# Optimization experiments

Hardware: AMD Instinct MI355X
Metric: run time of the kernel (lower is better)

The kernel has to match this reference:

```python
import jax, jax.numpy as jnp
import numpy as np

N, D = 8192, 128
NUM_CLASSES = 512
LA, UA, K, S, LAMBDA_G, MARGIN = 10.0, 110.0, 3.0, 30.0, 1.0, 0.0


def setup_inputs() -> dict:
    key = jax.random.key(0)
    k1, k2, k3 = jax.random.split(key, 3)
    feat = jax.random.normal(k1, (N, D), dtype=jnp.float32)
    uc = jax.random.uniform(k2, (N,), dtype=jnp.float32)
    label = jax.random.randint(k3, (N,), 0, NUM_CLASSES, dtype=jnp.int64)
    return {"feat": feat, "uc": uc, "label": label}


def _safe_sqrt(d2):
    # matches torch cdist subgradient: grad 0 at exactly-zero distance
    pos = d2 > 0
    return jnp.where(pos, jnp.sqrt(jnp.where(pos, d2, 1.0)), 0.0)


def reference(feat, uc, label):
    # --- norm regularizer g (reg_type='exp_3') ---
    norms = jnp.linalg.norm(feat, axis=-1)                      # [N]
    nx = (norms - LA) / (UA - LA)
    ug = 2.7183 ** (-K)
    reg = ((jnp.exp(-nx * K) / K + ug * nx) / (1.0 - ug)).mean() * LAMBDA_G

    mask = label[:, None] == label[None, :]                      # [N, N] bool

    # normalize=True branch: unit-normalize then euclidean cdist
    f = feat / jnp.maximum(norms, 1e-12)[:, None]                # F.normalize
    gram = f @ f.T                                               # [N, N]
    d2 = jnp.clip(2.0 - 2.0 * gram, 0.0, None)
    similarity = -_safe_sqrt(d2)                                 # -cdist

    uc_pair = uc[:, None] + uc[None, :]
    correction = jnp.where(mask, -(uc_pair - MARGIN), uc_pair)

    similarity = jnp.arcsin(similarity / 2.0) * 2.0 - correction # convert_dist

    maskf = mask.astype(similarity.dtype)
    nmaskf = 1.0 - maskf
    s_pos = -similarity * maskf - 10.0 * nmaskf
    s_neg = similarity * nmaskf - 10.0 * maskf

    logit_p = jax.nn.logsumexp(s_pos * S, axis=-1)               # [N]
    logit_n = jax.nn.logsumexp(s_neg * S, axis=-1)               # [N]
    loss = jax.nn.softplus(logit_p + logit_n).mean()

    # forward returns loss/s + (reg - reg.detach()) (value == loss/s)
    out = loss / S + (reg - jax.lax.stop_gradient(reg))
    return out
```

## Files before the change

### kernel.cpp

```cpp
#include <hip/hip_runtime.h>
#include <hip/hip_bf16.h>
#include <stdint.h>

#define N_ROWS 8192
#define DIM 128
#define NCLS 512
#define NCHUNK 16
#define CHUNK 512
#define JT 32
#define ROUNDS (CHUNK / JT)

#define S2D 43.2808512266689
#define PI2D 1.5707963267948966
#define CN 56.0f
#define CP 16.0f

typedef __attribute__((ext_vector_type(8))) short bf16x8;
typedef __attribute__((ext_vector_type(4))) float f32x4;


__device__ __forceinline__ unsigned short bf16_rne(float f) {
  uint32_t u = __float_as_uint(f);
  u += 0x7FFFu + ((u >> 16) & 1u);
  return (unsigned short)(u >> 16);
}
__device__ __forceinline__ float bf16_f(unsigned short h) {
  return __uint_as_float(((uint32_t)h) << 16);
}

__device__ __forceinline__ float acos_fast(float x) {
  float ax = fabsf(x);
  float p = fmaf(ax, -0.0012624911f, 0.0066700901f);
  p = fmaf(ax, p, -0.0170881256f);
  p = fmaf(ax, p, 0.0308918810f);
  p = fmaf(ax, p, -0.0501743046f);
  p = fmaf(ax, p, 0.0889789874f);
  p = fmaf(ax, p, -0.2145988016f);
  p = fmaf(ax, p, 1.5707963050f);
  float r = sqrtf(1.0f - ax) * p;
  return x >= 0.0f ? r : 3.14159265358979f - r;
}

__device__ __forceinline__ void gload16(const void* g, void* l) {
  __builtin_amdgcn_global_load_lds(
      (__attribute__((address_space(1))) void*)(void*)g,
      (__attribute__((address_space(3))) void*)l, 16, 0, 0);
}


__global__ __launch_bounds__(256) void prep_kernel(const float* __restrict__ feat,
                                                   const int* __restrict__ label,
                                                   unsigned short* __restrict__ fhi,
                                                   unsigned short* __restrict__ flo,
                                                   int* __restrict__ cls_start,
                                                   int* __restrict__ cls_idx) {
  __shared__ int cnt[NCLS];
  __shared__ int ofs[NCLS];
  const int t = threadIdx.x;
  const int w = t >> 6, l = t & 63;

  int row = blockIdx.x * 4 + w;
  float2 v = *(const float2*)(feat + (size_t)row * DIM + l * 2);
  float ss = v.x * v.x + v.y * v.y;
  #pragma unroll
  for (int m = 32; m; m >>= 1) ss += __shfl_xor(ss, m);
  float scale = 1.0f / fmaxf(sqrtf(ss), 1e-12f);
  float fx = v.x * scale, fy = v.y * scale;
  unsigned short hx = bf16_rne(fx), hy = bf16_rne(fy);
  unsigned short lx = bf16_rne(fx - bf16_f(hx)), ly = bf16_rne(fy - bf16_f(hy));
  *(ushort2*)(fhi + (size_t)row * DIM + l * 2) = make_ushort2(hx, hy);
  *(ushort2*)(flo + (size_t)row * DIM + l * 2) = make_ushort2(lx, ly);

  if (blockIdx.x == 0) {
    for (int i = t; i < NCLS; i += 256) cnt[i] = 0;
    __syncthreads();
    for (int i = t; i < N_ROWS; i += 256) atomicAdd(&cnt[label[i]], 1);
    __syncthreads();
    if (t < 64) {
      int loc[8];
      int base = 0;
      #pragma unroll
      for (int b = 0; b < 8; ++b) { loc[b] = base; base += cnt[l * 8 + b]; }
      int v2 = base;
      #pragma unroll
      for (int off = 1; off < 64; off <<= 1) {
        int n = __shfl_up(v2, off);
        if (l >= off) v2 += n;
      }
      int ex = v2 - base;
      #pragma unroll
      for (int b = 0; b < 8; ++b) {
        int s = ex + loc[b];
        ofs[l * 8 + b] = s;
        cls_start[l * 8 + b] = s;
      }
      if (l == 63) cls_start[NCLS] = ex + base;
    }
    __syncthreads();
    for (int i = t; i < N_ROWS; i += 256) {
      int c = label[i];
      int p = atomicAdd(&ofs[c], 1);
      cls_idx[p] = i;
    }
  }
}


__global__ __launch_bounds__(256, 5) void pair_kernel(const unsigned short* __restrict__ fhi,
                                                      const unsigned short* __restrict__ flo,
                                                      const float* __restrict__ uc,
                                                      const int* __restrict__ label,
                                                      float* __restrict__ partial) {
  __shared__ __attribute__((aligned(16))) char smem[2 * 16384];
  constexpr float S2 = (float)S2D;
  constexpr float S2PI2 = (float)(S2D * PI2D);
  constexpr float A0 = (float)(1.0 * S2D);
  constexpr float A1 = (float)(1.0 / 6.0 * S2D);
  constexpr float A2 = (float)(3.0 / 40.0 * S2D);
  constexpr float A3 = (float)(15.0 / 336.0 * S2D);
  constexpr float A4 = (float)(105.0 / 3456.0 * S2D);

  const int t = threadIdx.x;
  const int w = t >> 6, l = t & 63;
  const int lr = l & 15, lg = l >> 4;

  const int lin = blockIdx.y * 128 + blockIdx.x;
  const int dat = (lin & 7) * 256 + (lin >> 3);
  const int i0 = (dat & 127) * 64;
  const int chunk = dat >> 7;

  const char* fhb = (const char*)fhi;
  const char* flb = (const char*)flo;

  bf16x8 a_hi[4], a_lo[4];
  {
    int arow = i0 + w * 16 + lr;
    #pragma unroll
    for (int kk = 0; kk < 4; ++kk) {
      int off = arow * 256 + kk * 64 + lg * 16;
      a_hi[kk] = *(const bf16x8*)(fhb + off);
      a_lo[kk] = *(const bf16x8*)(flb + off);
    }
  }

  int li[4]; float K0[4];
  #pragma unroll
  for (int q = 0; q < 4; ++q) {
    int r = i0 + w * 16 + lg * 4 + q;
    li[q] = label[r];
    K0[q] = CN - S2PI2 - uc[r] * S2;
  }

  float sn[4] = {0.f, 0.f, 0.f, 0.f};

  const int sw = (lr & 7) << 4;
  const int bb = lr * 256 + ((lg * 16) ^ (sw & 0x30));
  int koff[4];
  #pragma unroll
  for (int kk = 0; kk < 4; ++kk) koff[kk] = (kk * 64) ^ (sw & 0x40);

  int rc[2];
  #pragma unroll
  for (int c = 0; c < 2; ++c) {
    int aoff = c * 4096 + t * 16;
    int row = aoff >> 8;
    int off = aoff & 255;
    rc[c] = row * 256 + (off ^ ((row & 7) << 4));
  }
  const int ldst = w * 1024;

  size_t goff = (size_t)chunk * CHUNK * 256;

  #pragma unroll
  for (int c = 0; c < 2; ++c) {
    gload16(fhb + goff + rc[c], smem + c * 4096 + ldst);
    gload16(flb + goff + rc[c], smem + 8192 + c * 4096 + ldst);
  }
  __syncthreads();

  int cur = 0;
  for (int r = 0; r < ROUNDS; ++r) {
    const int j0 = chunk * CHUNK + r * JT;
    int lj_r[2]; float us_r[2];
    #pragma unroll
    for (int sub = 0; sub < 2; ++sub) {
      int j = j0 + sub * 16 + lr;
      lj_r[sub] = label[j];
      us_r[sub] = uc[j] * S2;
    }
    if (r + 1 < ROUNDS) {
      char* nb = smem + (cur ^ 1) * 16384;
      size_t g2 = goff + JT * 256;
      #pragma unroll
      for (int c = 0; c < 2; ++c) {
        gload16(fhb + g2 + rc[c], nb + c * 4096 + ldst);
        gload16(flb + g2 + rc[c], nb + 8192 + c * 4096 + ldst);
      }
    }

    const char* cb_ = smem + cur * 16384;
    #pragma unroll
    for (int sub = 0; sub < 2; ++sub) {
      f32x4 aA = {0.f,0.f,0.f,0.f}, aB = {0.f,0.f,0.f,0.f}, aC = {0.f,0.f,0.f,0.f};
      #pragma unroll
      for (int kk = 0; kk < 4; ++kk) {
        const char* ba = cb_ + bb + koff[kk] + sub * 4096;
        bf16x8 bh = *(const bf16x8*)(ba);
        bf16x8 bl = *(const bf16x8*)(ba + 8192);
        aA = __builtin_amdgcn_mfma_f32_16x16x32_bf16(a_hi[kk], bh, aA, 0, 0, 0);
        aB = __builtin_amdgcn_mfma_f32_16x16x32_bf16(a_hi[kk], bl, aB, 0, 0, 0);
        aC = __builtin_amdgcn_mfma_f32_16x16x32_bf16(a_lo[kk], bh, aC, 0, 0, 0);
      }
      f32x4 acc = (aA + aB) + aC;

      const int lj = lj_r[sub];
      const float us = us_r[sub];
      #pragma unroll
      for (int q = 0; q < 4; ++q) {
        float g = acc[q];
        float u = g * g;
        float p = fmaf(u, A4, A3);
        p = fmaf(u, p, A2);
        p = fmaf(u, p, A1);
        p = fmaf(u, p, A0);
        float vn = fmaf(g, p, K0[q] - us);
        vn = (li[q] == lj) ? -1e30f : vn;
        sn[q] += __builtin_amdgcn_exp2f(vn);
      }
    }
    __syncthreads();
    goff += JT * 256;
    cur ^= 1;
  }

  #pragma unroll
  for (int q = 0; q < 4; ++q) {
    #pragma unroll
    for (int msk = 1; msk < 16; msk <<= 1) sn[q] += __shfl_xor(sn[q], msk);
  }
  if (lr == 0) {
    #pragma unroll
    for (int q = 0; q < 4; ++q) {
      int r = i0 + w * 16 + lg * 4 + q;
      partial[(size_t)r * NCHUNK + chunk] = sn[q];
    }
  }
}


__global__ __launch_bounds__(256) void finalize_kernel(const unsigned short* __restrict__ fhi,
                                                       const unsigned short* __restrict__ flo,
                                                       const float* __restrict__ uc,
                                                       const int* __restrict__ label,
                                                       const float* __restrict__ partial,
                                                       const int* __restrict__ cls_start,
                                                       const int* __restrict__ cls_idx,
                                                       float* __restrict__ blocksum) {
  constexpr float S2 = (float)S2D;
  __shared__ float wsum[4];
  const int t = threadIdx.x;
  const int w = t >> 6, l = t & 63;
  const int row = blockIdx.x * 4 + w;

  float sn = (l < NCHUNK) ? partial[(size_t)row * NCHUNK + l] : 0.f;
  #pragma unroll
  for (int m = 32; m; m >>= 1) sn += __shfl_xor(sn, m);

  ushort2 hi2 = *(const ushort2*)(fhi + (size_t)row * DIM + l * 2);
  ushort2 lo2 = *(const ushort2*)(flo + (size_t)row * DIM + l * 2);
  float fx = bf16_f(hi2.x) + bf16_f(lo2.x);
  float fy = bf16_f(hi2.y) + bf16_f(lo2.y);

  const int c = label[row];
  const int ks = cls_start[c], ke = cls_start[c + 1];
  const float uci = uc[row];
  float sp = 0.f;
  for (int k = ks; k < ke; ++k) {
    int j = cls_idx[k];
    ushort2 hj = *(const ushort2*)(fhi + (size_t)j * DIM + l * 2);
    ushort2 lj = *(const ushort2*)(flo + (size_t)j * DIM + l * 2);
    float g = fx * (bf16_f(hj.x) + bf16_f(lj.x)) + fy * (bf16_f(hj.y) + bf16_f(lj.y));
    #pragma unroll
    for (int m = 32; m; m >>= 1) g += __shfl_xor(g, m);
    g = fminf(1.0f, fmaxf(-1.0f, g));
    float th = acos_fast(g);
    float vp = fmaf(S2, th, -S2 * (uci + uc[j]) - CP);
    sp += __builtin_amdgcn_exp2f(vp);
  }

  float z2 = log2f(sp) + log2f(sn) + (CP - CN);
  float z = 0.69314718056f * z2;
  float v = (z > 20.f) ? z : log1pf(__expf(z));

  if (l == 0) wsum[w] = v;
  __syncthreads();
  if (t == 0) blocksum[blockIdx.x] = wsum[0] + wsum[1] + wsum[2] + wsum[3];
}


__global__ __launch_bounds__(256) void finalize2_kernel(const float* __restrict__ blocksum,
                                                        float* __restrict__ out) {
  __shared__ float w4[4];
  int t = threadIdx.x;
  float s = 0.f;
  #pragma unroll
  for (int k = 0; k < 8; ++k) s += blocksum[t + k * 256];
  #pragma unroll
  for (int m = 32; m; m >>= 1) s += __shfl_xor(s, m);
  if ((t & 63) == 0) w4[t >> 6] = s;
  __syncthreads();
  if (t == 0) out[0] = (w4[0] + w4[1] + w4[2] + w4[3]) * (1.0f / (8192.0f * 30.0f));
}


extern "C" void kernel_launch(void* const* d_in, const int* in_sizes, int n_in,
                              void* d_out, int out_size, void* d_ws, size_t ws_size,
                              hipStream_t stream) {
  const float* feat = (const float*)d_in[0];
  const float* uc   = (const float*)d_in[1];
  const int*   label = (const int*)d_in[2];
  float* out = (float*)d_out;
  char* ws = (char*)d_ws;

  unsigned short* fhi = (unsigned short*)ws;
  unsigned short* flo = (unsigned short*)(ws + (size_t)N_ROWS * DIM * 2);
  float* partial = (float*)(ws + (size_t)N_ROWS * DIM * 4);
  char* p2 = ws + (size_t)N_ROWS * DIM * 4 + (size_t)N_ROWS * NCHUNK * 4;
  int* cls_start = (int*)p2;
  int* cls_idx = (int*)(p2 + 2048 + 64);
  float* blocksum = (float*)(p2 + 2048 + 64 + 32768);

  prep_kernel<<<N_ROWS / 4, 256, 0, stream>>>(feat, label, fhi, flo, cls_start, cls_idx);
  pair_kernel<<<dim3(128, 16), 256, 0, stream>>>(fhi, flo, uc, label, partial);
  finalize_kernel<<<N_ROWS / 4, 256, 0, stream>>>(fhi, flo, uc, label, partial,
                                                  cls_start, cls_idx, blocksum);
  finalize2_kernel<<<1, 256, 0, stream>>>(blocksum, out);
}
```

Baseline: 167.9 us.

## Exploit pairwise symmetry: compute only lower-triangular tiles with column-sum atomics

The negative-pair term is symmetric in i and j, so the pair kernel now launches only tiles on or below the diagonal (1088 instead of 2048). Strictly off-diagonal tiles also reduce their exponentials across rows and atomically add them into a per-column sum, which finalize adds to each row's partial sums. This roughly halves the MFMA and exp work, but adds per-subtile shuffles, global atomics, a memset, and a load imbalance from the triangular tile mapping.

```diff
diff --git a/kernel.cpp b/kernel.cpp
--- a/kernel.cpp
+++ b/kernel.cpp
@@ -9,6 +9,7 @@
 #define CHUNK 512
 #define JT 32
 #define ROUNDS (CHUNK / JT)
+#define NTILES 1088
 
 #define S2D 43.2808512266689
 #define PI2D 1.5707963267948966
@@ -110,7 +111,8 @@
                                                       const unsigned short* __restrict__ flo,
                                                       const float* __restrict__ uc,
                                                       const int* __restrict__ label,
-                                                      float* __restrict__ partial) {
+                                                      float* __restrict__ partial,
+                                                      float* __restrict__ colsum) {
   __shared__ __attribute__((aligned(16))) char smem[2 * 16384];
   constexpr float S2 = (float)S2D;
   constexpr float S2PI2 = (float)(S2D * PI2D);
@@ -124,10 +126,16 @@
   const int w = t >> 6, l = t & 63;
   const int lr = l & 15, lg = l >> 4;
 
-  const int lin = blockIdx.y * 128 + blockIdx.x;
-  const int dat = (lin & 7) * 256 + (lin >> 3);
-  const int i0 = (dat & 127) * 64;
-  const int chunk = dat >> 7;
+  int c = 0;
+  {
+    int rem = blockIdx.x;
+    while (true) { int cnt = 128 - 8 * c; if (rem < cnt) break; rem -= cnt; ++c; }
+    c = (c << 16) | rem;
+  }
+  const int chunk = c >> 16;
+  const int t_ = 8 * chunk + (c & 0xFFFF);
+  const int i0 = t_ * 64;
+  const bool strict = (t_ >= 8 * chunk + 8);
 
   const char* fhb = (const char*)fhi;
   const char* flb = (const char*)flo;
@@ -161,20 +169,20 @@
 
   int rc[2];
   #pragma unroll
-  for (int c = 0; c < 2; ++c) {
-    int aoff = c * 4096 + t * 16;
+  for (int cc = 0; cc < 2; ++cc) {
+    int aoff = cc * 4096 + t * 16;
     int row = aoff >> 8;
     int off = aoff & 255;
-    rc[c] = row * 256 + (off ^ ((row & 7) << 4));
+    rc[cc] = row * 256 + (off ^ ((row & 7) << 4));
   }
   const int ldst = w * 1024;
 
   size_t goff = (size_t)chunk * CHUNK * 256;
 
   #pragma unroll
-  for (int c = 0; c < 2; ++c) {
-    gload16(fhb + goff + rc[c], smem + c * 4096 + ldst);
-    gload16(flb + goff + rc[c], smem + 8192 + c * 4096 + ldst);
+  for (int cc = 0; cc < 2; ++cc) {
+    gload16(fhb + goff + rc[cc], smem + cc * 4096 + ldst);
+    gload16(flb + goff + rc[cc], smem + 8192 + cc * 4096 + ldst);
   }
   __syncthreads();
 
@@ -192,9 +200,9 @@
       char* nb = smem + (cur ^ 1) * 16384;
       size_t g2 = goff + JT * 256;
       #pragma unroll
-      for (int c = 0; c < 2; ++c) {
-        gload16(fhb + g2 + rc[c], nb + c * 4096 + ldst);
-        gload16(flb + g2 + rc[c], nb + 8192 + c * 4096 + ldst);
+      for (int cc = 0; cc < 2; ++cc) {
+        gload16(fhb + g2 + rc[cc], nb + cc * 4096 + ldst);
+        gload16(flb + g2 + rc[cc], nb + 8192 + cc * 4096 + ldst);
       }
     }
 
@@ -215,6 +223,7 @@
 
       const int lj = lj_r[sub];
       const float us = us_r[sub];
+      float e[4];
       #pragma unroll
       for (int q = 0; q < 4; ++q) {
         float g = acc[q];
@@ -225,7 +234,14 @@
         p = fmaf(u, p, A0);
         float vn = fmaf(g, p, K0[q] - us);
         vn = (li[q] == lj) ? -1e30f : vn;
-        sn[q] += __builtin_amdgcn_exp2f(vn);
+        e[q] = __builtin_amdgcn_exp2f(vn);
+        sn[q] += e[q];
+      }
+      if (strict) {
+        float cs = (e[0] + e[1]) + (e[2] + e[3]);
+        cs += __shfl_xor(cs, 16);
+        cs += __shfl_xor(cs, 32);
+        if (l < 16) atomicAdd(&colsum[j0 + sub * 16 + l], cs);
       }
     }
     __syncthreads();
@@ -253,6 +269,7 @@
                                                        const float* __restrict__ uc,
                                                        const int* __restrict__ label,
                                                        const float* __restrict__ partial,
+                                                       const float* __restrict__ colsum,
                                                        const int* __restrict__ cls_start,
                                                        const int* __restrict__ cls_idx,
                                                        float* __restrict__ blocksum) {
@@ -261,10 +278,12 @@
   const int t = threadIdx.x;
   const int w = t >> 6, l = t & 63;
   const int row = blockIdx.x * 4 + w;
-
-  float sn = (l < NCHUNK) ? partial[(size_t)row * NCHUNK + l] : 0.f;
+  const int c_r = row >> 9;
+
+  float sn = (l <= c_r) ? partial[(size_t)row * NCHUNK + l] : 0.f;
   #pragma unroll
   for (int m = 32; m; m >>= 1) sn += __shfl_xor(sn, m);
+  sn += colsum[row];
 
   ushort2 hi2 = *(const ushort2*)(fhi + (size_t)row * DIM + l * 2);
   ushort2 lo2 = *(const ushort2*)(flo + (size_t)row * DIM + l * 2);
@@ -329,10 +348,12 @@
   int* cls_start = (int*)p2;
   int* cls_idx = (int*)(p2 + 2048 + 64);
   float* blocksum = (float*)(p2 + 2048 + 64 + 32768);
-
+  float* colsum = (float*)(p2 + 2048 + 64 + 32768 + 8192);
+
+  hipMemsetAsync(colsum, 0, N_ROWS * sizeof(float), stream);
   prep_kernel<<<N_ROWS / 4, 256, 0, stream>>>(feat, label, fhi, flo, cls_start, cls_idx);
-  pair_kernel<<<dim3(128, 16), 256, 0, stream>>>(fhi, flo, uc, label, partial);
-  finalize_kernel<<<N_ROWS / 4, 256, 0, stream>>>(fhi, flo, uc, label, partial,
+  pair_kernel<<<NTILES, 256, 0, stream>>>(fhi, flo, uc, label, partial, colsum);
+  finalize_kernel<<<N_ROWS / 4, 256, 0, stream>>>(fhi, flo, uc, label, partial, colsum,
                                                   cls_start, cls_idx, blocksum);
   finalize2_kernel<<<1, 256, 0, stream>>>(blocksum, out);
 }
```

Result: slower. 174.4 us (+3.9%).
